# Kernel tuning notes

Hardware: AMD Instinct MI355X
Metric: run time of the kernel (lower is better)

The kernel has to match this reference:

```python
import jax, jax.numpy as jnp
import numpy as np

D_MODEL = 1024
NUM_HEADS = 16
D_K = D_MODEL // NUM_HEADS
B, S = 2, 2048


def setup_inputs() -> dict:
    key = jax.random.key(0)
    ks = jax.random.split(key, 12)
    s = 1.0 / np.sqrt(D_MODEL)
    inp = {
        "Q": jax.random.normal(ks[0], (B, S, D_MODEL), jnp.float32),
        "K": jax.random.normal(ks[1], (B, S, D_MODEL), jnp.float32),
        "V": jax.random.normal(ks[2], (B, S, D_MODEL), jnp.float32),
        "mask": jnp.tril(jnp.ones((S, S), jnp.int32))[None, None],  # causal [1,1,S,S]
        "W_Q": jax.random.uniform(ks[3], (D_MODEL, D_MODEL), jnp.float32, -s, s),
        "b_Q": jax.random.uniform(ks[4], (D_MODEL,), jnp.float32, -s, s),
        "W_K": jax.random.uniform(ks[5], (D_MODEL, D_MODEL), jnp.float32, -s, s),
        "b_K": jax.random.uniform(ks[6], (D_MODEL,), jnp.float32, -s, s),
        "W_V": jax.random.uniform(ks[7], (D_MODEL, D_MODEL), jnp.float32, -s, s),
        "b_V": jax.random.uniform(ks[8], (D_MODEL,), jnp.float32, -s, s),
        "W_O": jax.random.uniform(ks[9], (D_MODEL, D_MODEL), jnp.float32, -s, s),
        "b_O": jax.random.uniform(ks[10], (D_MODEL,), jnp.float32, -s, s),
    }
    return inp


def _split_heads(x):
    b, s, _ = x.shape
    return x.reshape(b, s, NUM_HEADS, D_K).transpose(0, 2, 1, 3)  # [B,H,S,d_k]


def reference(Q, K, V, mask, W_Q, b_Q, W_K, b_K, W_V, b_V, W_O, b_O):
    q = _split_heads(Q @ W_Q.T + b_Q)
    k = _split_heads(K @ W_K.T + b_K)
    v = _split_heads(V @ W_V.T + b_V)
    scores = jnp.einsum("bhqd,bhkd->bhqk", q, k) / jnp.sqrt(jnp.float32(D_K))
    scores = jnp.where(mask == 0, -jnp.inf, scores)
    attn = jax.nn.softmax(scores, axis=-1)
    out = jnp.einsum("bhqk,bhkd->bhqd", attn, v)
    out = out.transpose(0, 2, 1, 3).reshape(Q.shape[0], Q.shape[1], D_MODEL)
    out = out @ W_O.T + b_O
    return out, attn
```

## Files before the change

### kernel.cpp

```cpp
#include <hip/hip_runtime.h>

typedef __attribute__((ext_vector_type(4))) float f32x4;
typedef __attribute__((ext_vector_type(8))) __bf16 bf16x8;
typedef __attribute__((ext_vector_type(4))) __bf16 bf16x4;

#define D_MODEL 1024
#define S_LEN 2048
#define MROWS 4096

#if __has_builtin(__builtin_amdgcn_exp2f)
#define EXP2F(x) __builtin_amdgcn_exp2f(x)
#else
#define EXP2F(x) exp2f(x)
#endif

#define QSCALE 0.1803368801111204f

__device__ __forceinline__ void gload_lds16(const void* g, void* l) {
  __builtin_amdgcn_global_load_lds(
      (const __attribute__((address_space(1))) unsigned int*)g,
      (__attribute__((address_space(3))) unsigned int*)l, 16, 0, 0);
}

__global__ void cvt_qkv(const float* __restrict__ Q, const float* __restrict__ K,
                        const float* __restrict__ V, __bf16* __restrict__ dst) {
  const int y = blockIdx.y;
  const float* src = (y == 0) ? Q : (y == 1) ? K : V;
  __bf16* d = dst + (size_t)y * (MROWS * D_MODEL);
  const int n4 = MROWS * D_MODEL / 4;
  for (int i = blockIdx.x * blockDim.x + threadIdx.x; i < n4; i += 512 * 256) {
    f32x4 v = *(const f32x4*)(src + i * 4);
    bf16x4 o;
#pragma unroll
    for (int j = 0; j < 4; ++j) o[j] = (__bf16)v[j];
    *(bf16x4*)(d + i * 4) = o;
  }
}

__global__ void cvt_w(const float* __restrict__ w0, const float* __restrict__ w1,
                      const float* __restrict__ w2, const float* __restrict__ w3,
                      __bf16* __restrict__ dst) {
  const int y = blockIdx.y;
  const float* src = (y == 0) ? w0 : (y == 1) ? w1 : (y == 2) ? w2 : w3;
  const float sc = (y == 0) ? QSCALE : 1.0f;
  __bf16* d = dst + (size_t)y * (D_MODEL * D_MODEL);
  const int n4 = D_MODEL * D_MODEL / 4;
  for (int i = blockIdx.x * blockDim.x + threadIdx.x; i < n4; i += 256 * 256) {
    f32x4 v = *(const f32x4*)(src + i * 4);
    bf16x4 o;
#pragma unroll
    for (int j = 0; j < 4; ++j) o[j] = (__bf16)(v[j] * sc);
    *(bf16x4*)(d + i * 4) = o;
  }
}

__device__ __forceinline__ void gemm_core64(const __bf16* __restrict__ A,
                                            const __bf16* __restrict__ B,
                                            __bf16* As, __bf16* Bs,
                                            int m0, int n0, f32x4 (&acc)[4][4]) {
  const int tid = threadIdx.x;
  const int lane = tid & 63, wid = tid >> 6;
  const int li = lane & 15, g = lane >> 4;
  const int wr = wid >> 1, wc = wid & 1;
  const int srow = tid >> 3, sc = tid & 7;
  const int scol = (sc ^ (srow & 7)) * 8;
  const int sw = li & 7;
  for (int k0 = 0; k0 < D_MODEL; k0 += 64) {
#pragma unroll
    for (int i = 0; i < 4; ++i) {
      const int r = i * 32 + srow;
      gload_lds16(A + (size_t)(m0 + r) * D_MODEL + k0 + scol, (char*)As + i * 4096 + wid * 1024);
      gload_lds16(B + (size_t)(n0 + r) * D_MODEL + k0 + scol, (char*)Bs + i * 4096 + wid * 1024);
    }
    __syncthreads();
#pragma unroll
    for (int kk = 0; kk < 2; ++kk) {
      bf16x8 af[4], bfr[4];
#pragma unroll
      for (int i = 0; i < 4; ++i) {
        af[i]  = *(const bf16x8*)&As[(wr * 64 + i * 16 + li) * 64 + (((kk * 4 + g) ^ sw) * 8)];
        bfr[i] = *(const bf16x8*)&Bs[(wc * 64 + i * 16 + li) * 64 + (((kk * 4 + g) ^ sw) * 8)];
      }
      __builtin_amdgcn_s_setprio(1);
#pragma unroll
      for (int i = 0; i < 4; ++i)
#pragma unroll
        for (int j = 0; j < 4; ++j)
          acc[i][j] = __builtin_amdgcn_mfma_f32_16x16x32_bf16(af[i], bfr[j], acc[i][j], 0, 0, 0);
      __builtin_amdgcn_s_setprio(0);
    }
    __syncthreads();
  }
}

__global__ __launch_bounds__(256) void qkv_gemm(
    const __bf16* __restrict__ Qb, const __bf16* __restrict__ Kb, const __bf16* __restrict__ Vb,
    const __bf16* __restrict__ Wq, const __bf16* __restrict__ Wk, const __bf16* __restrict__ Wv,
    const float* __restrict__ bq, const float* __restrict__ bk, const float* __restrict__ bv,
    __bf16* __restrict__ qp, __bf16* __restrict__ kp, __bf16* __restrict__ vt) {
  __shared__ __bf16 As[128 * 64];
  __shared__ __bf16 Bs[128 * 64];
  const int z = blockIdx.z;
  const __bf16* A = (z == 0) ? Qb : (z == 1) ? Kb : Vb;
  const __bf16* B = (z == 0) ? Wq : (z == 1) ? Wk : Wv;
  const float* bias = (z == 0) ? bq : (z == 1) ? bk : bv;
  const float bsc = (z == 0) ? QSCALE : 1.0f;
  const int m0 = blockIdx.x * 128, n0 = blockIdx.y * 128;
  f32x4 acc[4][4] = {};
  gemm_core64(A, B, As, Bs, m0, n0, acc);

  const int lane = threadIdx.x & 63, wid = threadIdx.x >> 6;
  const int li = lane & 15, g = lane >> 4;
  const int wr = wid >> 1, wc = wid & 1;
#pragma unroll
  for (int j = 0; j < 4; ++j) {
    const int n = n0 + wc * 64 + j * 16 + li;
    const float bv_ = bias[n] * bsc;
#pragma unroll
    for (int i = 0; i < 4; ++i) {
#pragma unroll
      for (int r = 0; r < 4; ++r) {
        const int m = m0 + wr * 64 + i * 16 + g * 4 + r;
        const float v = acc[i][j][r] + bv_;
        if (z == 2) {
          const int bb = m >> 11, s = m & 2047;
          vt[((size_t)(bb * D_MODEL + n)) * S_LEN + s] = (__bf16)v;
        } else {
          __bf16* o = (z == 0) ? qp : kp;
          o[(size_t)m * D_MODEL + n] = (__bf16)v;
        }
      }
    }
  }
}

__global__ __launch_bounds__(256) void o_gemm(const __bf16* __restrict__ ctx,
                                              const __bf16* __restrict__ Wo,
                                              const float* __restrict__ bo,
                                              float* __restrict__ out) {
  __shared__ __bf16 As[128 * 64];
  __shared__ __bf16 Bs[128 * 64];
  const int m0 = blockIdx.x * 128, n0 = blockIdx.y * 128;
  f32x4 acc[4][4] = {};
  gemm_core64(ctx, Wo, As, Bs, m0, n0, acc);

  const int lane = threadIdx.x & 63, wid = threadIdx.x >> 6;
  const int li = lane & 15, g = lane >> 4;
  const int wr = wid >> 1, wc = wid & 1;
#pragma unroll
  for (int j = 0; j < 4; ++j) {
    const int n = n0 + wc * 64 + j * 16 + li;
    const float bv_ = bo[n];
#pragma unroll
    for (int i = 0; i < 4; ++i)
#pragma unroll
      for (int r = 0; r < 4; ++r) {
        const int m = m0 + wr * 64 + i * 16 + g * 4 + r;
        out[(size_t)m * D_MODEL + n] = acc[i][j][r] + bv_;
      }
  }
}

__global__ __launch_bounds__(512, 4) void attn_fused4(const __bf16* __restrict__ qp,
                                                      const __bf16* __restrict__ kp,
                                                      const __bf16* __restrict__ vt,
                                                      float* __restrict__ attn,
                                                      __bf16* __restrict__ ctx) {
  const int bid = blockIdx.x;
  const int qt = 15 - (bid >> 5);
  const int bh = bid & 31;
  const int b = bh >> 4, h = bh & 15;
  const int tid = threadIdx.x, lane = tid & 63, wid = tid >> 6;
  const int li = lane & 15, g = lane >> 4;
  const int sw = li & 7;
  const int qrow0 = qt * 128 + wid * 16;
  const float NEG_INF = -__builtin_inff();

  __shared__ __bf16 k_lds[2][64 * 64];
  __shared__ __bf16 v_lds[2][64 * 64];
  __shared__ __bf16 p_lds[8][16 * 64];

  const __bf16* qbase = qp + ((size_t)(b * S_LEN + qrow0 + li)) * D_MODEL + h * 64 + g * 8;
  const bf16x8 qf0 = *(const bf16x8*)qbase;
  const bf16x8 qf1 = *(const bf16x8*)(qbase + 32);

  const int srow = tid >> 3;
  const int sc = tid & 7;
  const int schunk = (sc ^ (srow & 7)) * 8;
  const __bf16* kpb = kp + (size_t)(b * S_LEN) * D_MODEL + h * 64 + schunk;
  const __bf16* vpb = vt + (size_t)(bh * 64) * S_LEN + schunk;

  auto stage_k = [&](int kt, int bufi) {
    gload_lds16(kpb + (size_t)(kt * 64 + srow) * D_MODEL, (char*)k_lds[bufi] + wid * 1024);
  };
  auto stage_v = [&](int kt, int bufi) {
    gload_lds16(vpb + (size_t)srow * S_LEN + kt * 64, (char*)v_lds[bufi] + wid * 1024);
  };
  auto qk_tile = [&](const __bf16* kb, f32x4 (&sv)[4]) {
    __builtin_amdgcn_s_setprio(1);
#pragma unroll
    for (int sub = 0; sub < 4; ++sub) {
      const __bf16* rp = kb + (sub * 16 + li) * 64;
      const bf16x8 k0 = *(const bf16x8*)(rp + ((g ^ sw) * 8));
      const bf16x8 k1 = *(const bf16x8*)(rp + (((4 + g) ^ sw) * 8));
      f32x4 t = {};
      t = __builtin_amdgcn_mfma_f32_16x16x32_bf16(qf0, k0, t, 0, 0, 0);
      t = __builtin_amdgcn_mfma_f32_16x16x32_bf16(qf1, k1, t, 0, 0, 0);
      sv[sub] = t;
    }
    __builtin_amdgcn_s_setprio(0);
  };

  const int ktmax_w = 2 * qt + ((wid >= 4) ? 1 : 0);
  const int kt_end = 2 * qt + 1;

  float esum[4] = {0.f, 0.f, 0.f, 0.f};
  int buf = 0;
  stage_k(0, 0);
  for (int kt = 0; kt <= kt_end; ++kt) {
    __syncthreads();
    stage_k(kt + 1, buf ^ 1);
    if (kt <= ktmax_w) {
      f32x4 sv[4];
      qk_tile(k_lds[buf], sv);
      if (kt == ktmax_w) {
        const int rowl = qrow0 + g * 4;
#pragma unroll
        for (int sub = 0; sub < 4; ++sub) {
          const int col = kt * 64 + sub * 16 + li;
#pragma unroll
          for (int r = 0; r < 4; ++r)
            if (col > rowl + r) sv[sub][r] = NEG_INF;
        }
      }
#pragma unroll
      for (int r = 0; r < 4; ++r)
        esum[r] += (EXP2F(sv[0][r]) + EXP2F(sv[1][r])) + (EXP2F(sv[2][r]) + EXP2F(sv[3][r]));
    }
    buf ^= 1;
  }
  float inv_l[4];
#pragma unroll
  for (int r = 0; r < 4; ++r) {
    float e = esum[r];
    e += __shfl_xor(e, 1);
    e += __shfl_xor(e, 2);
    e += __shfl_xor(e, 4);
    e += __shfl_xor(e, 8);
    inv_l[r] = 1.f / e;
  }

  float* attn_bh = attn + (size_t)bh * S_LEN * S_LEN;
  float* arp[4];
#pragma unroll
  for (int r = 0; r < 4; ++r)
    arp[r] = attn_bh + (size_t)(qrow0 + g * 4 + r) * S_LEN + li;

  __bf16* pw = &p_lds[wid][0];
  f32x4 acc[4] = {};

  __syncthreads();
  buf = 0;
  stage_k(0, 0);
  stage_v(0, 0);
  for (int kt = 0; kt <= kt_end; ++kt) {
    __syncthreads();
    stage_k(kt + 1, buf ^ 1);
    stage_v(kt + 1, buf ^ 1);
    if (kt <= ktmax_w) {
      f32x4 sv[4];
      qk_tile(k_lds[buf], sv);
      if (kt == ktmax_w) {
        const int rowl = qrow0 + g * 4;
#pragma unroll
        for (int sub = 0; sub < 4; ++sub) {
          const int col = kt * 64 + sub * 16 + li;
#pragma unroll
          for (int r = 0; r < 4; ++r)
            if (col > rowl + r) sv[sub][r] = NEG_INF;
        }
      }
      const int colbase = kt * 64;
#pragma unroll
      for (int r = 0; r < 4; ++r) {
        const int prow = g * 4 + r;
#pragma unroll
        for (int sub = 0; sub < 4; ++sub) {
          const float p = EXP2F(sv[sub][r]) * inv_l[r];
          arp[r][colbase + sub * 16] = p;
          pw[prow * 64 + (((sub * 2 + (li >> 3)) ^ (prow & 7)) * 8) + (li & 7)] = (__bf16)p;
        }
      }
      __builtin_amdgcn_s_setprio(1);
      const bf16x8 pa0 = *(const bf16x8*)&pw[li * 64 + ((g ^ sw) * 8)];
      const bf16x8 pa1 = *(const bf16x8*)&pw[li * 64 + (((4 + g) ^ sw) * 8)];
      const __bf16* vb = v_lds[buf];
#pragma unroll
      for (int c4 = 0; c4 < 4; ++c4) {
        const __bf16* vrp = vb + (c4 * 16 + li) * 64;
        const bf16x8 vf0 = *(const bf16x8*)(vrp + ((g ^ sw) * 8));
        const bf16x8 vf1 = *(const bf16x8*)(vrp + (((4 + g) ^ sw) * 8));
        acc[c4] = __builtin_amdgcn_mfma_f32_16x16x32_bf16(pa0, vf0, acc[c4], 0, 0, 0);
        acc[c4] = __builtin_amdgcn_mfma_f32_16x16x32_bf16(pa1, vf1, acc[c4], 0, 0, 0);
      }
      __builtin_amdgcn_s_setprio(0);
    }
    buf ^= 1;
  }

#pragma unroll
  for (int c4 = 0; c4 < 4; ++c4)
#pragma unroll
    for (int r = 0; r < 4; ++r)
      ctx[((size_t)(b * S_LEN) + qrow0 + g * 4 + r) * D_MODEL + h * 64 + c4 * 16 + li] =
          (__bf16)acc[c4][r];

  const int c0 = (ktmax_w + 1) * 64;
  for (int r = 0; r < 16; ++r) {
    float* rowp = attn_bh + (size_t)(qrow0 + r) * S_LEN;
    for (int col = c0 + lane * 4; col < S_LEN; col += 256) {
      f32x4 z = {};
      *(f32x4*)(rowp + col) = z;
    }
  }
}

extern "C" void kernel_launch(void* const* d_in, const int* in_sizes, int n_in,
                              void* d_out, int out_size, void* d_ws, size_t ws_size,
                              hipStream_t stream) {
  const float* Q  = (const float*)d_in[0];
  const float* K  = (const float*)d_in[1];
  const float* V  = (const float*)d_in[2];
  const float* W_Q = (const float*)d_in[4];
  const float* b_Q = (const float*)d_in[5];
  const float* W_K = (const float*)d_in[6];
  const float* b_K = (const float*)d_in[7];
  const float* W_V = (const float*)d_in[8];
  const float* b_V = (const float*)d_in[9];
  const float* W_O = (const float*)d_in[10];
  const float* b_O = (const float*)d_in[11];

  char* ws = (char*)d_ws;
  __bf16* Qb  = (__bf16*)(ws + 0);
  __bf16* Wq  = (__bf16*)(ws + 25165824);
  __bf16* qp  = (__bf16*)(ws + 33554432);
  __bf16* kp  = (__bf16*)(ws + 41943040);
  __bf16* vtb = (__bf16*)(ws + 50331648);
  __bf16* ctx = (__bf16*)(ws + 58720256);
  __bf16* Kb = Qb + (size_t)MROWS * D_MODEL;
  __bf16* Vb = Kb + (size_t)MROWS * D_MODEL;
  __bf16* Wk = Wq + (size_t)D_MODEL * D_MODEL;
  __bf16* Wv = Wk + (size_t)D_MODEL * D_MODEL;
  __bf16* Wo = Wv + (size_t)D_MODEL * D_MODEL;

  float* out = (float*)d_out;
  float* attn = out + (size_t)MROWS * D_MODEL;

  cvt_qkv<<<dim3(512, 3), 256, 0, stream>>>(Q, K, V, Qb);
  cvt_w<<<dim3(256, 4), 256, 0, stream>>>(W_Q, W_K, W_V, W_O, Wq);

  qkv_gemm<<<dim3(32, 8, 3), 256, 0, stream>>>(Qb, Kb, Vb, Wq, Wk, Wv,
                                               b_Q, b_K, b_V, qp, kp, vtb);

  attn_fused4<<<512, 512, 0, stream>>>(qp, kp, vtb, attn, ctx);

  o_gemm<<<dim3(32, 8), 256, 0, stream>>>(ctx, Wo, b_O, out);
}
```

Baseline: 253.8 us.

## Shrink attention blocks to 64 query rows and stage two K tiles per sync

The fused attention kernel now uses 256-thread blocks that each own 64 query rows, launched as 1024 blocks instead of 512. Every wave in a block now handles the same number of key tiles, so the per-wave skipping on the causal diagonal goes away. The masking becomes a shared diagonal helper. The first softmax-sum pass loads and processes two K tiles per barrier from a 4-slot LDS buffer, which halves its synchronisations. The trade-offs are more blocks and more total K/V reloads across blocks, in return for finer-grained causal load balance and less idle wave time.

After: 253.6 us. About the same (-0.1%).

```diff
diff --git a/kernel.cpp b/kernel.cpp
--- a/kernel.cpp
+++ b/kernel.cpp
@@ -161,24 +161,23 @@
   }
 }
 
-__global__ __launch_bounds__(512, 4) void attn_fused4(const __bf16* __restrict__ qp,
-                                                      const __bf16* __restrict__ kp,
-                                                      const __bf16* __restrict__ vt,
-                                                      float* __restrict__ attn,
-                                                      __bf16* __restrict__ ctx) {
+__global__ __launch_bounds__(256) void attn_fused5(const __bf16* __restrict__ qp,
+                                                   const __bf16* __restrict__ kp,
+                                                   const __bf16* __restrict__ vt,
+                                                   float* __restrict__ attn,
+                                                   __bf16* __restrict__ ctx) {
   const int bid = blockIdx.x;
-  const int qt = 15 - (bid >> 5);
+  const int qt = 31 - (bid >> 5);
   const int bh = bid & 31;
   const int b = bh >> 4, h = bh & 15;
   const int tid = threadIdx.x, lane = tid & 63, wid = tid >> 6;
   const int li = lane & 15, g = lane >> 4;
   const int sw = li & 7;
-  const int qrow0 = qt * 128 + wid * 16;
+  const int qrow0 = qt * 64 + wid * 16;
   const float NEG_INF = -__builtin_inff();
 
-  __shared__ __bf16 k_lds[2][64 * 64];
-  __shared__ __bf16 v_lds[2][64 * 64];
-  __shared__ __bf16 p_lds[8][16 * 64];
+  __shared__ __bf16 kv_lds[4][64 * 64];
+  __shared__ __bf16 p_lds[4][16 * 64];
 
   const __bf16* qbase = qp + ((size_t)(b * S_LEN + qrow0 + li)) * D_MODEL + h * 64 + g * 8;
   const bf16x8 qf0 = *(const bf16x8*)qbase;
@@ -191,10 +190,16 @@
   const __bf16* vpb = vt + (size_t)(bh * 64) * S_LEN + schunk;
 
   auto stage_k = [&](int kt, int bufi) {
-    gload_lds16(kpb + (size_t)(kt * 64 + srow) * D_MODEL, (char*)k_lds[bufi] + wid * 1024);
+#pragma unroll
+    for (int i = 0; i < 2; ++i)
+      gload_lds16(kpb + (size_t)(kt * 64 + i * 32 + srow) * D_MODEL,
+                  (char*)kv_lds[bufi] + i * 4096 + wid * 1024);
   };
   auto stage_v = [&](int kt, int bufi) {
-    gload_lds16(vpb + (size_t)srow * S_LEN + kt * 64, (char*)v_lds[bufi] + wid * 1024);
+#pragma unroll
+    for (int i = 0; i < 2; ++i)
+      gload_lds16(vpb + (size_t)(i * 32 + srow) * S_LEN + kt * 64,
+                  (char*)kv_lds[2 + bufi] + i * 4096 + wid * 1024);
   };
   auto qk_tile = [&](const __bf16* kb, f32x4 (&sv)[4]) {
     __builtin_amdgcn_s_setprio(1);
@@ -210,34 +215,44 @@
     }
     __builtin_amdgcn_s_setprio(0);
   };
-
-  const int ktmax_w = 2 * qt + ((wid >= 4) ? 1 : 0);
-  const int kt_end = 2 * qt + 1;
+  const int rowl = wid * 16 + g * 4;
+  auto mask_diag = [&](f32x4 (&sv)[4]) {
+#pragma unroll
+    for (int sub = 0; sub < 4; ++sub) {
+      const int coll = sub * 16 + li;
+#pragma unroll
+      for (int r = 0; r < 4; ++r)
+        if (coll > rowl + r) sv[sub][r] = NEG_INF;
+    }
+  };
+
+  const int nt = qt + 1;
 
   float esum[4] = {0.f, 0.f, 0.f, 0.f};
-  int buf = 0;
   stage_k(0, 0);
-  for (int kt = 0; kt <= kt_end; ++kt) {
+  if (nt > 1) stage_k(1, 1);
+  for (int p0 = 0; p0 < nt; p0 += 2) {
+    const int cs = (p0 >> 1) & 1;
     __syncthreads();
-    stage_k(kt + 1, buf ^ 1);
-    if (kt <= ktmax_w) {
+    const int ns = cs ^ 1;
+    if (p0 + 2 < nt) stage_k(p0 + 2, ns * 2);
+    if (p0 + 3 < nt) stage_k(p0 + 3, ns * 2 + 1);
+    {
       f32x4 sv[4];
-      qk_tile(k_lds[buf], sv);
-      if (kt == ktmax_w) {
-        const int rowl = qrow0 + g * 4;
-#pragma unroll
-        for (int sub = 0; sub < 4; ++sub) {
-          const int col = kt * 64 + sub * 16 + li;
-#pragma unroll
-          for (int r = 0; r < 4; ++r)
-            if (col > rowl + r) sv[sub][r] = NEG_INF;
-        }
-      }
+      qk_tile(kv_lds[cs * 2], sv);
+      if (p0 == qt) mask_diag(sv);
 #pragma unroll
       for (int r = 0; r < 4; ++r)
         esum[r] += (EXP2F(sv[0][r]) + EXP2F(sv[1][r])) + (EXP2F(sv[2][r]) + EXP2F(sv[3][r]));
     }
-    buf ^= 1;
+    if (p0 + 1 < nt) {
+      f32x4 sv[4];
+      qk_tile(kv_lds[cs * 2 + 1], sv);
+      if (p0 + 1 == qt) mask_diag(sv);
+#pragma unroll
+      for (int r = 0; r < 4; ++r)
+        esum[r] += (EXP2F(sv[0][r]) + EXP2F(sv[1][r])) + (EXP2F(sv[2][r]) + EXP2F(sv[3][r]));
+    }
   }
   float inv_l[4];
 #pragma unroll
@@ -260,51 +275,40 @@
   f32x4 acc[4] = {};
 
   __syncthreads();
-  buf = 0;
+  int buf = 0;
   stage_k(0, 0);
   stage_v(0, 0);
-  for (int kt = 0; kt <= kt_end; ++kt) {
+  for (int kt = 0; kt < nt; ++kt) {
     __syncthreads();
     stage_k(kt + 1, buf ^ 1);
     stage_v(kt + 1, buf ^ 1);
-    if (kt <= ktmax_w) {
-      f32x4 sv[4];
-      qk_tile(k_lds[buf], sv);
-      if (kt == ktmax_w) {
-        const int rowl = qrow0 + g * 4;
-#pragma unroll
-        for (int sub = 0; sub < 4; ++sub) {
-          const int col = kt * 64 + sub * 16 + li;
-#pragma unroll
-          for (int r = 0; r < 4; ++r)
-            if (col > rowl + r) sv[sub][r] = NEG_INF;
-        }
+    f32x4 sv[4];
+    qk_tile(kv_lds[buf], sv);
+    if (kt == qt) mask_diag(sv);
+    const int colbase = kt * 64;
+#pragma unroll
+    for (int r = 0; r < 4; ++r) {
+      const int prow = g * 4 + r;
+#pragma unroll
+      for (int sub = 0; sub < 4; ++sub) {
+        const float p = EXP2F(sv[sub][r]) * inv_l[r];
+        arp[r][colbase + sub * 16] = p;
+        pw[prow * 64 + (((sub * 2 + (li >> 3)) ^ (prow & 7)) * 8) + (li & 7)] = (__bf16)p;
       }
-      const int colbase = kt * 64;
-#pragma unroll
-      for (int r = 0; r < 4; ++r) {
-        const int prow = g * 4 + r;
-#pragma unroll
-        for (int sub = 0; sub < 4; ++sub) {
-          const float p = EXP2F(sv[sub][r]) * inv_l[r];
-          arp[r][colbase + sub * 16] = p;
-          pw[prow * 64 + (((sub * 2 + (li >> 3)) ^ (prow & 7)) * 8) + (li & 7)] = (__bf16)p;
-        }
-      }
-      __builtin_amdgcn_s_setprio(1);
-      const bf16x8 pa0 = *(const bf16x8*)&pw[li * 64 + ((g ^ sw) * 8)];
-      const bf16x8 pa1 = *(const bf16x8*)&pw[li * 64 + (((4 + g) ^ sw) * 8)];
-      const __bf16* vb = v_lds[buf];
-#pragma unroll
-      for (int c4 = 0; c4 < 4; ++c4) {
-        const __bf16* vrp = vb + (c4 * 16 + li) * 64;
-        const bf16x8 vf0 = *(const bf16x8*)(vrp + ((g ^ sw) * 8));
-        const bf16x8 vf1 = *(const bf16x8*)(vrp + (((4 + g) ^ sw) * 8));
-        acc[c4] = __builtin_amdgcn_mfma_f32_16x16x32_bf16(pa0, vf0, acc[c4], 0, 0, 0);
-        acc[c4] = __builtin_amdgcn_mfma_f32_16x16x32_bf16(pa1, vf1, acc[c4], 0, 0, 0);
-      }
-      __builtin_amdgcn_s_setprio(0);
-    }
+    }
+    __builtin_amdgcn_s_setprio(1);
+    const bf16x8 pa0 = *(const bf16x8*)&pw[li * 64 + ((g ^ sw) * 8)];
+    const bf16x8 pa1 = *(const bf16x8*)&pw[li * 64 + (((4 + g) ^ sw) * 8)];
+    const __bf16* vb = kv_lds[2 + buf];
+#pragma unroll
+    for (int c4 = 0; c4 < 4; ++c4) {
+      const __bf16* vrp = vb + (c4 * 16 + li) * 64;
+      const bf16x8 vf0 = *(const bf16x8*)(vrp + ((g ^ sw) * 8));
+      const bf16x8 vf1 = *(const bf16x8*)(vrp + (((4 + g) ^ sw) * 8));
+      acc[c4] = __builtin_amdgcn_mfma_f32_16x16x32_bf16(pa0, vf0, acc[c4], 0, 0, 0);
+      acc[c4] = __builtin_amdgcn_mfma_f32_16x16x32_bf16(pa1, vf1, acc[c4], 0, 0, 0);
+    }
+    __builtin_amdgcn_s_setprio(0);
     buf ^= 1;
   }
 
@@ -315,7 +319,7 @@
       ctx[((size_t)(b * S_LEN) + qrow0 + g * 4 + r) * D_MODEL + h * 64 + c4 * 16 + li] =
           (__bf16)acc[c4][r];
 
-  const int c0 = (ktmax_w + 1) * 64;
+  const int c0 = nt * 64;
   for (int r = 0; r < 16; ++r) {
     float* rowp = attn_bh + (size_t)(qrow0 + r) * S_LEN;
     for (int col = c0 + lane * 4; col < S_LEN; col += 256) {
@@ -362,7 +366,7 @@
   qkv_gemm<<<dim3(32, 8, 3), 256, 0, stream>>>(Qb, Kb, Vb, Wq, Wk, Wv,
                                                b_Q, b_K, b_V, qp, kp, vtb);
 
-  attn_fused4<<<512, 512, 0, stream>>>(qp, kp, vtb, attn, ctx);
+  attn_fused5<<<1024, 256, 0, stream>>>(qp, kp, vtb, attn, ctx);
 
   o_gemm<<<dim3(32, 8), 256, 0, stream>>>(ctx, Wo, b_O, out);
 }
```
